# Kernel optimization log

Measured on AMD Instinct MI355X. Metric: run time of the kernel, lower is better.

Reference implementation:

```python
import jax, jax.numpy as jnp
import numpy as np

N = 100000      # nodes
E = 1600000     # edges
DIN = 128       # dim_in
H = 4           # heads
D = 16          # dim_out per head


def setup_inputs() -> dict:
    key = jax.random.key(0)
    k1, k2, k3, k4 = jax.random.split(key, 4)
    x = jax.random.normal(k1, (N, DIN), dtype=jnp.float32)
    edge_index = jax.random.randint(k2, (2, E), 0, N, dtype=jnp.int64)
    W_lin = jax.random.normal(k3, (DIN, H * D), dtype=jnp.float32) * 0.05
    W_att = jax.random.normal(k4, (H, 2 * D), dtype=jnp.float32) * 0.05
    return {"x": x, "edge_index": edge_index, "W_lin": W_lin, "W_att": W_att}


def reference(x, edge_index, W_lin, W_att):
    # node transform: [N, DIN] @ [DIN, H*D] -> [N, H, D]
    h = (x @ W_lin).reshape(-1, H, D)
    s, d = edge_index[0], edge_index[1]
    x_i = h[s]                                  # [E, H, D] (source / segment key)
    x_j = h[d]                                  # [E, H, D] (message source)
    x_ij = jnp.concatenate([x_i, x_j], axis=-1)  # [E, H, 2D]
    # per-head attention logit: e[e,h] = leaky_relu(<x_ij[e,h,:], W_att[h,:]>)
    e = jax.nn.leaky_relu(jnp.einsum('ehd,hd->eh', x_ij, W_att), 0.2)
    # numerically-stable segment softmax over source node s
    m = jax.ops.segment_max(e, s, num_segments=N)       # [N, H]
    ex = jnp.exp(e - m[s])                               # [E, H]
    denom = jax.ops.segment_sum(ex, s, num_segments=N)  # [N, H]
    alpha = ex / (denom[s] + 1e-16)                      # [E, H]
    # weighted scatter-add aggregation
    out = jax.ops.segment_sum(alpha[..., None] * x_j, s, num_segments=N)  # [N, H, D]
    return out.reshape(N, H * D)  # concat=True
```

## Files before the change

### kernel.cpp

```cpp
#include <hip/hip_runtime.h>


#define DIN 128
#define HD  64
#define NH  4
#define BTP 136
#define NB  1024
#define BSH 9

typedef __attribute__((ext_vector_type(8))) short short8;
typedef __attribute__((ext_vector_type(4))) float f32x4;

__device__ __forceinline__ float leaky02(float v) { return v > 0.f ? v : 0.2f * v; }

__device__ __forceinline__ float bf2f(unsigned short u) {
  union { unsigned u32; float f; } c; c.u32 = ((unsigned)u) << 16; return c.f;
}
__device__ __forceinline__ unsigned short f2bf(float f) {
  union { float f; unsigned u; } c; c.f = f;
  unsigned r = c.u + 0x7FFFu + ((c.u >> 16) & 1u);
  return (unsigned short)(r >> 16);
}
__device__ __forceinline__ unsigned cvt_pk_bf16(float lo, float hi) {
  unsigned r;
  asm("v_cvt_pk_bf16_f32 %0, %1, %2" : "=v"(r) : "v"(lo), "v"(hi));
  return r;
}

__global__ void k_wprep(const float* __restrict__ Wlin, const float* __restrict__ Watt,
                        unsigned short* __restrict__ btg) {
  for (int i = threadIdx.x; i < 80 * BTP; i += 256) {
    const int c = i / BTP, k = i % BTP;
    unsigned short v = 0;
    if (k < DIN) {
      if (c < 64) {
        v = f2bf(Wlin[k * HD + c]);
      } else if (c < 72) {
        const int cc = c - 64;
        const int head = cc & 3, dsth = (cc >= 4) ? 16 : 0;
        float s = 0.f;
#pragma unroll
        for (int d = 0; d < 16; ++d)
          s += Wlin[k * HD + head * 16 + d] * Watt[head * 32 + dsth + d];
        v = f2bf(s);
      }
    }
    btg[i] = v;
  }
}

__global__ __launch_bounds__(512)
void k_linear(const float* __restrict__ x,
              const unsigned short* __restrict__ btg,
              unsigned short* __restrict__ hb,
              float* __restrict__ a_src, float* __restrict__ a_dst,
              int N) {
  __shared__ __align__(16) unsigned short OT[8][16 * 68];
  __shared__ __align__(16) float AT[8][16 * 8];
  const int tid = threadIdx.x;
  const int lane = tid & 63;
  const int wid  = tid >> 6;

  const int row0 = blockIdx.x * 128 + wid * 16;
  if (row0 >= N) return;

  float4 xv[8];
  {
    const int r = min(row0 + (lane & 15), N - 1);
    const float* xp = x + (size_t)r * DIN + ((lane >> 4) * 8);
#pragma unroll
    for (int kt = 0; kt < 4; ++kt) {
      xv[kt * 2 + 0] = *(const float4*)(xp + kt * 32);
      xv[kt * 2 + 1] = *(const float4*)(xp + kt * 32 + 4);
    }
  }

  short8 bf[5][4];
#pragma unroll
  for (int ct = 0; ct < 5; ++ct) {
    const int c = (ct < 4) ? (ct * 16 + (lane & 15)) : (64 + (lane & 15));
#pragma unroll
    for (int kt = 0; kt < 4; ++kt)
      bf[ct][kt] = *(const short8*)(&btg[c * BTP + kt * 32 + (lane >> 4) * 8]);
  }

  short8 af[4];
#pragma unroll
  for (int kt = 0; kt < 4; ++kt) {
    unsigned* ap = (unsigned*)&af[kt];
    const float4 a = xv[kt * 2], b = xv[kt * 2 + 1];
    ap[0] = cvt_pk_bf16(a.x, a.y);
    ap[1] = cvt_pk_bf16(a.z, a.w);
    ap[2] = cvt_pk_bf16(b.x, b.y);
    ap[3] = cvt_pk_bf16(b.z, b.w);
  }
  f32x4 acc[5] = {{0,0,0,0},{0,0,0,0},{0,0,0,0},{0,0,0,0},{0,0,0,0}};
#pragma unroll
  for (int ct = 0; ct < 5; ++ct)
#pragma unroll
    for (int kt = 0; kt < 4; ++kt)
      acc[ct] = __builtin_amdgcn_mfma_f32_16x16x32_bf16(af[kt], bf[ct][kt], acc[ct], 0, 0, 0);

  const int c0 = lane & 15;
  const int r0 = (lane >> 4) * 4;
#pragma unroll
  for (int j = 0; j < 4; ++j) {
#pragma unroll
    for (int ct = 0; ct < 4; ++ct)
      OT[wid][(r0 + j) * 68 + ct * 16 + c0] = f2bf(acc[ct][j]);
    if (c0 < 8) AT[wid][(r0 + j) * 8 + c0] = acc[4][j];
  }
  unsigned* hbu = (unsigned*)(hb + (size_t)row0 * HD);
#pragma unroll
  for (int it = 0; it < 8; ++it) {
    const int rr = it * 2 + (lane >> 5);
    const int cw = lane & 31;
    const unsigned v = *(const unsigned*)&OT[wid][rr * 68 + cw * 2];
    if (row0 + rr < N) hbu[rr * 32 + cw] = v;
  }
  {
    const int rr = lane >> 2, cc = lane & 3;
    if (row0 + rr < N) {
      a_src[(row0 + rr) * 4 + cc] = AT[wid][rr * 8 + cc];
      a_dst[(row0 + rr) * 4 + cc] = AT[wid][rr * 8 + 4 + cc];
    }
  }
}

__global__ __launch_bounds__(256)
void k_p1(const int* __restrict__ ei, int* __restrict__ bhistT, int E, int B) {
  __shared__ unsigned lh[256];
  const int tid = threadIdx.x, blk = blockIdx.x;
  lh[tid] = 0;
  __syncthreads();
  const int per = (E + NB - 1) / NB;
  const int e0 = blk * per, e1 = min(e0 + per, E);
  for (int e = e0 + tid; e < e1; e += 256)
    atomicAdd(&lh[ei[e] >> BSH], 1u);
  __syncthreads();
  if (tid < B) bhistT[tid * NB + blk] = (int)lh[tid];
}

__global__ void k_scanA(const int* __restrict__ deg, int* __restrict__ offs,
                        int* __restrict__ partials, int N) {
  __shared__ int wsum[16];
  const int tid = threadIdx.x, lane = tid & 63, wv = tid >> 6;
  int i = blockIdx.x * 1024 + tid;
  int v = (i < N) ? deg[i] : 0;
  int sc = v;
#pragma unroll
  for (int s = 1; s < 64; s <<= 1) {
    int t = __shfl_up(sc, s, 64);
    if (lane >= s) sc += t;
  }
  if (lane == 63) wsum[wv] = sc;
  __syncthreads();
  if (wv == 0 && lane < 16) {
    int w = wsum[lane];
    int s2 = w;
#pragma unroll
    for (int s = 1; s < 16; s <<= 1) {
      int t = __shfl_up(s2, s, 64);
      if (lane >= s) s2 += t;
    }
    wsum[lane] = s2 - w;
  }
  __syncthreads();
  int excl = sc - v + wsum[wv];
  if (i < N) offs[i] = excl;
  if (tid == 1023) partials[blockIdx.x] = excl + v;
}

__global__ void k_scanB(int* __restrict__ offs, const int* __restrict__ partials, int N) {
  __shared__ int sbase;
  const int tid = threadIdx.x, b = blockIdx.x;
  if (tid < 64) {
    int acc = 0;
    for (int j = tid; j < b; j += 64) acc += partials[j];
#pragma unroll
    for (int s = 32; s >= 1; s >>= 1) acc += __shfl_xor(acc, s, 64);
    if (tid == 0) sbase = acc;
  }
  __syncthreads();
  int i = b * 1024 + tid;
  if (i < N) offs[i] += sbase;
}

__global__ __launch_bounds__(256)
void k_p3(const int* __restrict__ ei, const int* __restrict__ sbase,
          unsigned long long* __restrict__ tmp, int E) {
  __shared__ unsigned lh[256];
  const int tid = threadIdx.x, blk = blockIdx.x;
  lh[tid] = 0;
  __syncthreads();
  const int per = (E + NB - 1) / NB;
  const int e0 = blk * per, e1 = min(e0 + per, E);
  for (int e = e0 + tid; e < e1; e += 256) {
    const int s = ei[e];
    const int d = ei[E + e];
    const int b = s >> BSH;
    const unsigned lr = atomicAdd(&lh[b], 1u);
    const int pos = sbase[b * NB + blk] + (int)lr;
    tmp[pos] = ((unsigned long long)(unsigned)s << 32) | (unsigned)d;
  }
}

__global__ __launch_bounds__(256)
void k_p4(const unsigned long long* __restrict__ tmp, const int* __restrict__ sbase,
          int* __restrict__ deg, int* __restrict__ offs, int* __restrict__ csr,
          int E, int N, int B) {
  __shared__ unsigned lh[512];
  __shared__ unsigned ex[512];
  __shared__ unsigned run[512];
  const int tid = threadIdx.x, b = blockIdx.x;
  const int lo = b << BSH;
  const int start = sbase[b * NB];
  const int end = (b + 1 < B) ? sbase[(b + 1) * NB] : E;

  lh[tid] = 0; lh[tid + 256] = 0;
  __syncthreads();
  for (int i = start + tid; i < end; i += 256)
    atomicAdd(&lh[(unsigned)(tmp[i] >> 32) - lo], 1u);
  __syncthreads();

  if (tid < 64) {
    const int lane = tid;
    unsigned carry = 0;
#pragma unroll
    for (int c = 0; c < 8; ++c) {
      unsigned v = lh[c * 64 + lane];
      unsigned sc = v;
#pragma unroll
      for (int sft = 1; sft < 64; sft <<= 1) {
        unsigned t = __shfl_up(sc, sft, 64);
        if (lane >= sft) sc += t;
      }
      ex[c * 64 + lane] = sc - v + carry;
      carry += __shfl(sc, 63, 64);
    }
  }
  __syncthreads();

  for (int i = tid; i < 512; i += 256) {
    const int n = lo + i;
    if (n < N) {
      deg[n]  = (int)lh[i];
      offs[n] = start + (int)ex[i];
    }
    run[i] = ex[i];
  }
  __syncthreads();

  for (int i = start + tid; i < end; i += 256) {
    const unsigned long long p = tmp[i];
    const unsigned s = (unsigned)(p >> 32);
    const unsigned r = atomicAdd(&run[s - lo], 1u);
    csr[start + (int)r] = (int)(unsigned)p;
  }
}

__global__ __launch_bounds__(256)
void k_agg(const int* __restrict__ offs_start, const int* __restrict__ deg,
           const int* __restrict__ csr, const float4* __restrict__ a_src4,
           const float4* __restrict__ a_dst4,
           const unsigned short* __restrict__ hb,
           float* __restrict__ out, int N) {
  __shared__ float als[4][64 * NH];
  const int lane = threadIdx.x & 63;
  const int wid  = threadIdx.x >> 6;
  const int hh = lane >> 4;
  const int wstride = gridDim.x * 4;

  for (int n0 = blockIdx.x * 4 + wid; n0 < N; n0 += wstride) {
    const int n   = __builtin_amdgcn_readfirstlane(n0);
    const int beg = __builtin_amdgcn_readfirstlane(offs_start[n]);
    const int dg  = __builtin_amdgcn_readfirstlane(deg[n]);
    const int end = beg + dg;
    const float4 asv = a_src4[n];

    float s0 = 0.f, s1 = 0.f, s2 = 0.f, s3 = 0.f;
    float acc0 = 0.f, acc1 = 0.f;
    for (int base = beg; base < end; base += 64) {
      const int cnt = __builtin_amdgcn_readfirstlane(min(64, end - base));
      const bool act = lane < cnt;
      const int d = csr[act ? base + lane : beg];
      const float4 ad = a_dst4[d];
      const float p0 = act ? __expf(leaky02(asv.x + ad.x)) : 0.f;
      const float p1 = act ? __expf(leaky02(asv.y + ad.y)) : 0.f;
      const float p2 = act ? __expf(leaky02(asv.z + ad.z)) : 0.f;
      const float p3 = act ? __expf(leaky02(asv.w + ad.w)) : 0.f;
      s0 += p0; s1 += p1; s2 += p2; s3 += p3;
      *(float4*)&als[wid][lane * 4] = make_float4(p0, p1, p2, p3);

      int j = 0;
      for (; j + 8 <= cnt; j += 8) {
        int dds[8];
#pragma unroll
        for (int u = 0; u < 8; ++u)
          dds[u] = __builtin_amdgcn_readfirstlane(csr[base + j + u]);
        float hv[8];
#pragma unroll
        for (int u = 0; u < 8; ++u) hv[u] = bf2f(hb[(size_t)dds[u] * HD + lane]);
#pragma unroll
        for (int u = 0; u < 8; ++u) {
          const float av = als[wid][(j + u) * 4 + hh];
          if (u & 1) acc1 = fmaf(av, hv[u], acc1);
          else       acc0 = fmaf(av, hv[u], acc0);
        }
      }
      for (; j < cnt; ++j) {
        const int dd_ = __builtin_amdgcn_readfirstlane(csr[base + j]);
        const float av = als[wid][j * 4 + hh];
        acc0 = fmaf(av, bf2f(hb[(size_t)dd_ * HD + lane]), acc0);
      }
    }
#pragma unroll
    for (int s = 1; s < 64; s <<= 1) {
      s0 += __shfl_xor(s0, s, 64); s1 += __shfl_xor(s1, s, 64);
      s2 += __shfl_xor(s2, s, 64); s3 += __shfl_xor(s3, s, 64);
    }
    const float sh = (hh == 0) ? s0 : (hh == 1) ? s1 : (hh == 2) ? s2 : s3;
    out[(size_t)n * HD + lane] = (acc0 + acc1) * (1.f / (sh + 1e-16f));
  }
}

extern "C" void kernel_launch(void* const* d_in, const int* in_sizes, int n_in,
                              void* d_out, int out_size, void* d_ws, size_t ws_size,
                              hipStream_t stream) {
  const float* x    = (const float*)d_in[0];
  const int*   ei   = (const int*)d_in[1];
  const float* Wlin = (const float*)d_in[2];
  const float* Watt = (const float*)d_in[3];
  float* out = (float*)d_out;

  const int N = in_sizes[0] / DIN;
  const int E = in_sizes[1] / 2;
  const int B = (N + (1 << BSH) - 1) >> BSH;
  const int M = B * NB;

  char* ws = (char*)d_ws;
  size_t off = 0;
  auto align16 = [&off]() { off = (off + 15) & ~(size_t)15; };
  unsigned short* hb = (unsigned short*)(ws + off); off += (size_t)N * HD * sizeof(unsigned short); align16();
  float* a_src  = (float*)(ws + off); off += (size_t)N * NH * sizeof(float); align16();
  float* a_dst  = (float*)(ws + off); off += (size_t)N * NH * sizeof(float); align16();
  int*   deg    = (int*)(ws + off);   off += (size_t)N * sizeof(int); align16();
  int*   offs   = (int*)(ws + off);   off += ((size_t)N + 1) * sizeof(int); align16();
  int*   csr    = (int*)(ws + off);   off += (size_t)E * sizeof(int); align16();
  unsigned long long* tmp = (unsigned long long*)(ws + off); off += (size_t)E * sizeof(unsigned long long); align16();
  int*   bhistT = (int*)(ws + off);   off += (size_t)M * sizeof(int); align16();
  int*   sbase  = (int*)(ws + off);   off += (size_t)M * sizeof(int); align16();
  int*   parts  = (int*)(ws + off);   off += 256 * sizeof(int); align16();
  unsigned short* btg = (unsigned short*)(ws + off); off += 80 * BTP * sizeof(unsigned short); align16();

  hipLaunchKernelGGL(k_wprep, dim3(1), dim3(256), 0, stream, Wlin, Watt, btg);

  hipLaunchKernelGGL(k_linear, dim3((N + 127) / 128), dim3(512), 0, stream,
                     x, btg, hb, a_src, a_dst, N);

  hipLaunchKernelGGL(k_p1, dim3(NB), dim3(256), 0, stream, ei, bhistT, E, B);

  const int SB = (M + 1023) / 1024;
  hipLaunchKernelGGL(k_scanA, dim3(SB), dim3(1024), 0, stream, bhistT, sbase, parts, M);
  hipLaunchKernelGGL(k_scanB, dim3(SB), dim3(1024), 0, stream, sbase, parts, M);

  hipLaunchKernelGGL(k_p3, dim3(NB), dim3(256), 0, stream, ei, sbase, tmp, E);

  hipLaunchKernelGGL(k_p4, dim3(B), dim3(256), 0, stream,
                     tmp, sbase, deg, offs, csr, E, N, B);

  hipLaunchKernelGGL(k_agg, dim3(4096), dim3(256), 0, stream,
                     offs, deg, csr, (const float4*)a_src, (const float4*)a_dst, hb, out, N);
}
```

Measured before the change: 143.7 us.

## Fuse source-bucket histogram into linear kernel and unroll aggregation gather by 16

Moves the edge-bucket histogram pass into the node-transform kernel, so each of the nb=(N+127)/128 linear blocks also counts its slice of source indices, removing one kernel launch. The partition count now follows the linear grid (~782 instead of 1024), so the scan sizes, p3 grid and p4 indexing are changed to match. The aggregation loop also gains a 16-wide unrolled gather stage ahead of the 8-wide one to put more loads in flight. This risks higher register pressure in k_agg and fewer, larger histogram/scatter blocks.

```diff
diff --git a/kernel.cpp b/kernel.cpp
--- a/kernel.cpp
+++ b/kernel.cpp
@@ -5,7 +5,6 @@
 #define HD  64
 #define NH  4
 #define BTP 136
-#define NB  1024
 #define BSH 9
 
 typedef __attribute__((ext_vector_type(8))) short short8;
@@ -54,91 +53,93 @@
               const unsigned short* __restrict__ btg,
               unsigned short* __restrict__ hb,
               float* __restrict__ a_src, float* __restrict__ a_dst,
-              int N) {
+              int N,
+              const int* __restrict__ ei, int* __restrict__ bhistT,
+              int E, int B, int nb) {
   __shared__ __align__(16) unsigned short OT[8][16 * 68];
   __shared__ __align__(16) float AT[8][16 * 8];
+  __shared__ unsigned lh[256];
   const int tid = threadIdx.x;
   const int lane = tid & 63;
   const int wid  = tid >> 6;
 
+  if (tid < 256) lh[tid] = 0;
+
   const int row0 = blockIdx.x * 128 + wid * 16;
-  if (row0 >= N) return;
-
-  float4 xv[8];
-  {
-    const int r = min(row0 + (lane & 15), N - 1);
-    const float* xp = x + (size_t)r * DIN + ((lane >> 4) * 8);
+  const bool rowok = row0 < N;
+
+  if (rowok) {
+    float4 xv[8];
+    {
+      const int r = min(row0 + (lane & 15), N - 1);
+      const float* xp = x + (size_t)r * DIN + ((lane >> 4) * 8);
+#pragma unroll
+      for (int kt = 0; kt < 4; ++kt) {
+        xv[kt * 2 + 0] = *(const float4*)(xp + kt * 32);
+        xv[kt * 2 + 1] = *(const float4*)(xp + kt * 32 + 4);
+      }
+    }
+
+    short8 bf[5][4];
+#pragma unroll
+    for (int ct = 0; ct < 5; ++ct) {
+      const int c = (ct < 4) ? (ct * 16 + (lane & 15)) : (64 + (lane & 15));
+#pragma unroll
+      for (int kt = 0; kt < 4; ++kt)
+        bf[ct][kt] = *(const short8*)(&btg[c * BTP + kt * 32 + (lane >> 4) * 8]);
+    }
+
+    short8 af[4];
 #pragma unroll
     for (int kt = 0; kt < 4; ++kt) {
-      xv[kt * 2 + 0] = *(const float4*)(xp + kt * 32);
-      xv[kt * 2 + 1] = *(const float4*)(xp + kt * 32 + 4);
-    }
-  }
-
-  short8 bf[5][4];
-#pragma unroll
-  for (int ct = 0; ct < 5; ++ct) {
-    const int c = (ct < 4) ? (ct * 16 + (lane & 15)) : (64 + (lane & 15));
-#pragma unroll
-    for (int kt = 0; kt < 4; ++kt)
-      bf[ct][kt] = *(const short8*)(&btg[c * BTP + kt * 32 + (lane >> 4) * 8]);
-  }
-
-  short8 af[4];
-#pragma unroll
-  for (int kt = 0; kt < 4; ++kt) {
-    unsigned* ap = (unsigned*)&af[kt];
-    const float4 a = xv[kt * 2], b = xv[kt * 2 + 1];
-    ap[0] = cvt_pk_bf16(a.x, a.y);
-    ap[1] = cvt_pk_bf16(a.z, a.w);
-    ap[2] = cvt_pk_bf16(b.x, b.y);
-    ap[3] = cvt_pk_bf16(b.z, b.w);
-  }
-  f32x4 acc[5] = {{0,0,0,0},{0,0,0,0},{0,0,0,0},{0,0,0,0},{0,0,0,0}};
-#pragma unroll
-  for (int ct = 0; ct < 5; ++ct)
-#pragma unroll
-    for (int kt = 0; kt < 4; ++kt)
-      acc[ct] = __builtin_amdgcn_mfma_f32_16x16x32_bf16(af[kt], bf[ct][kt], acc[ct], 0, 0, 0);
-
-  const int c0 = lane & 15;
-  const int r0 = (lane >> 4) * 4;
-#pragma unroll
-  for (int j = 0; j < 4; ++j) {
-#pragma unroll
-    for (int ct = 0; ct < 4; ++ct)
-      OT[wid][(r0 + j) * 68 + ct * 16 + c0] = f2bf(acc[ct][j]);
-    if (c0 < 8) AT[wid][(r0 + j) * 8 + c0] = acc[4][j];
-  }
-  unsigned* hbu = (unsigned*)(hb + (size_t)row0 * HD);
-#pragma unroll
-  for (int it = 0; it < 8; ++it) {
-    const int rr = it * 2 + (lane >> 5);
-    const int cw = lane & 31;
-    const unsigned v = *(const unsigned*)&OT[wid][rr * 68 + cw * 2];
-    if (row0 + rr < N) hbu[rr * 32 + cw] = v;
-  }
-  {
-    const int rr = lane >> 2, cc = lane & 3;
-    if (row0 + rr < N) {
-      a_src[(row0 + rr) * 4 + cc] = AT[wid][rr * 8 + cc];
-      a_dst[(row0 + rr) * 4 + cc] = AT[wid][rr * 8 + 4 + cc];
-    }
-  }
-}
-
-__global__ __launch_bounds__(256)
-void k_p1(const int* __restrict__ ei, int* __restrict__ bhistT, int E, int B) {
-  __shared__ unsigned lh[256];
-  const int tid = threadIdx.x, blk = blockIdx.x;
-  lh[tid] = 0;
-  __syncthreads();
-  const int per = (E + NB - 1) / NB;
-  const int e0 = blk * per, e1 = min(e0 + per, E);
-  for (int e = e0 + tid; e < e1; e += 256)
+      unsigned* ap = (unsigned*)&af[kt];
+      const float4 a = xv[kt * 2], b = xv[kt * 2 + 1];
+      ap[0] = cvt_pk_bf16(a.x, a.y);
+      ap[1] = cvt_pk_bf16(a.z, a.w);
+      ap[2] = cvt_pk_bf16(b.x, b.y);
+      ap[3] = cvt_pk_bf16(b.z, b.w);
+    }
+    f32x4 acc[5] = {{0,0,0,0},{0,0,0,0},{0,0,0,0},{0,0,0,0},{0,0,0,0}};
+#pragma unroll
+    for (int ct = 0; ct < 5; ++ct)
+#pragma unroll
+      for (int kt = 0; kt < 4; ++kt)
+        acc[ct] = __builtin_amdgcn_mfma_f32_16x16x32_bf16(af[kt], bf[ct][kt], acc[ct], 0, 0, 0);
+
+    const int c0 = lane & 15;
+    const int r0 = (lane >> 4) * 4;
+#pragma unroll
+    for (int j = 0; j < 4; ++j) {
+#pragma unroll
+      for (int ct = 0; ct < 4; ++ct)
+        OT[wid][(r0 + j) * 68 + ct * 16 + c0] = f2bf(acc[ct][j]);
+      if (c0 < 8) AT[wid][(r0 + j) * 8 + c0] = acc[4][j];
+    }
+    unsigned* hbu = (unsigned*)(hb + (size_t)row0 * HD);
+#pragma unroll
+    for (int it = 0; it < 8; ++it) {
+      const int rr = it * 2 + (lane >> 5);
+      const int cw = lane & 31;
+      const unsigned v = *(const unsigned*)&OT[wid][rr * 68 + cw * 2];
+      if (row0 + rr < N) hbu[rr * 32 + cw] = v;
+    }
+    {
+      const int rr = lane >> 2, cc = lane & 3;
+      if (row0 + rr < N) {
+        a_src[(row0 + rr) * 4 + cc] = AT[wid][rr * 8 + cc];
+        a_dst[(row0 + rr) * 4 + cc] = AT[wid][rr * 8 + 4 + cc];
+      }
+    }
+  }
+
+  __syncthreads();
+  const int per = (E + nb - 1) / nb;
+  const int e0 = blockIdx.x * per;
+  const int e1 = min(e0 + per, E);
+  for (int e = e0 + tid; e < e1; e += 512)
     atomicAdd(&lh[ei[e] >> BSH], 1u);
   __syncthreads();
-  if (tid < B) bhistT[tid * NB + blk] = (int)lh[tid];
+  if (tid < B) bhistT[tid * nb + blockIdx.x] = (int)lh[tid];
 }
 
 __global__ void k_scanA(const int* __restrict__ deg, int* __restrict__ offs,
@@ -188,19 +189,19 @@
 
 __global__ __launch_bounds__(256)
 void k_p3(const int* __restrict__ ei, const int* __restrict__ sbase,
-          unsigned long long* __restrict__ tmp, int E) {
+          unsigned long long* __restrict__ tmp, int E, int nb) {
   __shared__ unsigned lh[256];
   const int tid = threadIdx.x, blk = blockIdx.x;
   lh[tid] = 0;
   __syncthreads();
-  const int per = (E + NB - 1) / NB;
+  const int per = (E + nb - 1) / nb;
   const int e0 = blk * per, e1 = min(e0 + per, E);
   for (int e = e0 + tid; e < e1; e += 256) {
     const int s = ei[e];
     const int d = ei[E + e];
     const int b = s >> BSH;
     const unsigned lr = atomicAdd(&lh[b], 1u);
-    const int pos = sbase[b * NB + blk] + (int)lr;
+    const int pos = sbase[b * nb + blk] + (int)lr;
     tmp[pos] = ((unsigned long long)(unsigned)s << 32) | (unsigned)d;
   }
 }
@@ -208,14 +209,14 @@
 __global__ __launch_bounds__(256)
 void k_p4(const unsigned long long* __restrict__ tmp, const int* __restrict__ sbase,
           int* __restrict__ deg, int* __restrict__ offs, int* __restrict__ csr,
-          int E, int N, int B) {
+          int E, int N, int B, int nb) {
   __shared__ unsigned lh[512];
   __shared__ unsigned ex[512];
   __shared__ unsigned run[512];
   const int tid = threadIdx.x, b = blockIdx.x;
   const int lo = b << BSH;
-  const int start = sbase[b * NB];
-  const int end = (b + 1 < B) ? sbase[(b + 1) * NB] : E;
+  const int start = sbase[b * nb];
+  const int end = (b + 1 < B) ? sbase[(b + 1) * nb] : E;
 
   lh[tid] = 0; lh[tid + 256] = 0;
   __syncthreads();
@@ -293,6 +294,21 @@
       *(float4*)&als[wid][lane * 4] = make_float4(p0, p1, p2, p3);
 
       int j = 0;
+      for (; j + 16 <= cnt; j += 16) {
+        int dds[16];
+#pragma unroll
+        for (int u = 0; u < 16; ++u)
+          dds[u] = __builtin_amdgcn_readfirstlane(csr[base + j + u]);
+        float hv[16];
+#pragma unroll
+        for (int u = 0; u < 16; ++u) hv[u] = bf2f(hb[(size_t)dds[u] * HD + lane]);
+#pragma unroll
+        for (int u = 0; u < 16; ++u) {
+          const float av = als[wid][(j + u) * 4 + hh];
+          if (u & 1) acc1 = fmaf(av, hv[u], acc1);
+          else       acc0 = fmaf(av, hv[u], acc0);
+        }
+      }
       for (; j + 8 <= cnt; j += 8) {
         int dds[8];
 #pragma unroll
@@ -336,7 +352,8 @@
   const int N = in_sizes[0] / DIN;
   const int E = in_sizes[1] / 2;
   const int B = (N + (1 << BSH) - 1) >> BSH;
-  const int M = B * NB;
+  const int nb = (N + 127) / 128;
+  const int M = B * nb;
 
   char* ws = (char*)d_ws;
   size_t off = 0;
@@ -355,19 +372,17 @@
 
   hipLaunchKernelGGL(k_wprep, dim3(1), dim3(256), 0, stream, Wlin, Watt, btg);
 
-  hipLaunchKernelGGL(k_linear, dim3((N + 127) / 128), dim3(512), 0, stream,
-                     x, btg, hb, a_src, a_dst, N);
-
-  hipLaunchKernelGGL(k_p1, dim3(NB), dim3(256), 0, stream, ei, bhistT, E, B);
+  hipLaunchKernelGGL(k_linear, dim3(nb), dim3(512), 0, stream,
+                     x, btg, hb, a_src, a_dst, N, ei, bhistT, E, B, nb);
 
   const int SB = (M + 1023) / 1024;
   hipLaunchKernelGGL(k_scanA, dim3(SB), dim3(1024), 0, stream, bhistT, sbase, parts, M);
   hipLaunchKernelGGL(k_scanB, dim3(SB), dim3(1024), 0, stream, sbase, parts, M);
 
-  hipLaunchKernelGGL(k_p3, dim3(NB), dim3(256), 0, stream, ei, sbase, tmp, E);
+  hipLaunchKernelGGL(k_p3, dim3(nb), dim3(256), 0, stream, ei, sbase, tmp, E, nb);
 
   hipLaunchKernelGGL(k_p4, dim3(B), dim3(256), 0, stream,
-                     tmp, sbase, deg, offs, csr, E, N, B);
+                     tmp, sbase, deg, offs, csr, E, N, B, nb);
 
   hipLaunchKernelGGL(k_agg, dim3(4096), dim3(256), 0, stream,
                      offs, deg, csr, (const float4*)a_src, (const float4*)a_dst, hb, out, N);
```

Result: slower. 151.9 us (+5.7%).
